# Kernel tuning notes

Measured on AMD Instinct MI355X. Metric: run time of the kernel, lower is better.

The kernel has to match this reference:

```python
import jax, jax.numpy as jnp
import numpy as np

N = 50000  # nodes
E = 800000  # edges (avg degree 16)


def gcn_agg(x, senders, receivers, n, add_self_edges):
    """jraph.GraphConvolution aggregation with symmetric normalization.
    x: [n, d] node feats already passed through update_node_fn."""
    if add_self_edges:
        idx = jnp.arange(n, dtype=senders.dtype)
        s = jnp.concatenate([senders, idx])
        r = jnp.concatenate([receivers, idx])
    else:
        s, r = senders, receivers
    ones = jnp.ones(s.shape, x.dtype)
    sdeg = jax.ops.segment_sum(ones, s, num_segments=n)
    rdeg = jax.ops.segment_sum(ones, r, num_segments=n)
    x = x * jax.lax.rsqrt(jnp.maximum(sdeg, 1.0))[:, None]
    x = jax.ops.segment_sum(x[s], r, num_segments=n)  # [E+,d] gather -> scatter-sum
    return x * jax.lax.rsqrt(jnp.maximum(rdeg, 1.0))[:, None]


def setup_inputs() -> dict:
    key = jax.random.key(0)
    ks = jax.random.split(key, 9)
    d_in, d_h, d_z, d_out = 128, 128, 64, 128

    def w(k, i, o):
        return jax.random.normal(k, (i, o), jnp.float32) / np.float32(np.sqrt(i))

    return {
        "nodes": jax.random.normal(ks[0], (N, d_in), jnp.float32),
        "senders": jax.random.randint(ks[1], (E,), 0, N, jnp.int32),
        "receivers": jax.random.randint(ks[2], (E,), 0, N, jnp.int32),
        "eps": jax.random.normal(ks[3], (N, d_z), jnp.float32),
        "W_h": w(ks[4], d_in, d_h), "b_h": jnp.zeros((d_h,), jnp.float32),
        "W_mu": w(ks[5], d_h, d_z), "b_mu": jnp.zeros((d_z,), jnp.float32),
        "W_ls": w(ks[6], d_h, d_z), "b_ls": jnp.zeros((d_z,), jnp.float32),
        "W_dh": w(ks[7], d_z, d_h), "b_dh": jnp.zeros((d_h,), jnp.float32),
        "W_do": w(ks[8], d_h, d_out), "b_do": jnp.zeros((d_out,), jnp.float32),
    }


def reference(nodes, senders, receivers, eps, W_h, b_h, W_mu, b_mu,
              W_ls, b_ls, W_dh, b_dh, W_do, b_do):
    n = nodes.shape[0]
    # encoder hidden GCN (add_self_edges=True): Linear+elu update, then agg.
    # (the first of the two identical encoder GCN calls in the source is dead
    #  code -- both read the original graph, only the 2nd result is used)
    h = jax.nn.elu(nodes @ W_h + b_h)
    h = gcn_agg(h, senders, receivers, n, True)
    # mean / log_std GCNs (add_self_edges=False)
    mean = gcn_agg(h @ W_mu + b_mu, senders, receivers, n, False)
    log_std = gcn_agg(h @ W_ls + b_ls, senders, receivers, n, False)
    # reparameterization
    z = mean + jnp.exp(log_std) * eps
    # decoder: GCN(self edges, Linear+elu) -> GCN(no self edges, Linear)
    d = jax.nn.elu(z @ W_dh + b_dh)
    d = gcn_agg(d, senders, receivers, n, True)
    out = gcn_agg(d @ W_do + b_do, senders, receivers, n, False)
    return mean, log_std, out
```

## Files before the change

kernel.cpp:

```cpp
#include <hip/hip_runtime.h>
#include <hip/hip_bf16.h>
#include <hip/hip_fp16.h>
#include <math.h>


typedef _Float16 f16x8 __attribute__((ext_vector_type(8)));
typedef float    f32x4 __attribute__((ext_vector_type(4)));

#define HSL 64
#define HIST_LDS_W 12544
#define NSLICE 256
#define CAP 8000

__global__ __launch_bounds__(256)
void hist8s_k(const int* __restrict__ snd, unsigned int* __restrict__ partial,
              int nE, int nW)
{
    __shared__ unsigned int sh[HIST_LDS_W];
    const int slice = blockIdx.x;
    for (int w = threadIdx.x; w < nW; w += 256) sh[w] = 0u;
    __syncthreads();
    const int per = (nE + HSL - 1) / HSL;
    const int e1 = min(nE, slice * per + per);
    for (int e = slice * per + threadIdx.x; e < e1; e += 256) {
        int v = snd[e];
        atomicAdd(&sh[v >> 2], 1u << ((v & 3) * 8));
    }
    __syncthreads();
    unsigned int* dst = partial + (size_t)slice * nW;
    for (int w = threadIdx.x; w < nW; w += 256) dst[w] = sh[w];
}

__global__ __launch_bounds__(256)
void hist8s_reduce_k(const unsigned int* __restrict__ partial,
                     float* __restrict__ dsi, float* __restrict__ dsn,
                     int n, int nW)
{
    int w = blockIdx.x * 256 + threadIdx.x;
    if (w >= nW) return;
    const unsigned int* src = partial + w;
    int c0 = 0, c1 = 0, c2 = 0, c3 = 0;
    for (int s = 0; s < HSL; ++s) {
        unsigned int v = src[(size_t)s * nW];
        c0 += v & 255u; c1 += (v >> 8) & 255u; c2 += (v >> 16) & 255u; c3 += v >> 24;
    }
    const int cc[4] = {c0, c1, c2, c3};
    const int node0 = w * 4;
#pragma unroll
    for (int u = 0; u < 4; ++u) {
        int node = node0 + u;
        if (node >= n) break;
        float fd = (float)cc[u];
        dsi[node] = rsqrtf(fd + 1.0f);
        dsn[node] = rsqrtf(fmaxf(fd, 1.0f));
    }
}

__global__ __launch_bounds__(256)
void rcount_k(const int* __restrict__ rcv, int* __restrict__ cnt, int nE, int nb)
{
    __shared__ int lc[256];
    const int s = blockIdx.x;
    if (threadIdx.x < nb) lc[threadIdx.x] = 0;
    __syncthreads();
    const int per = (nE + NSLICE - 1) / NSLICE;
    const int e1 = min(nE, (s + 1) * per);
    for (int e = s * per + threadIdx.x; e < e1; e += 256)
        atomicAdd(&lc[rcv[e] >> 8], 1);
    __syncthreads();
    if (threadIdx.x < nb) cnt[s * nb + threadIdx.x] = lc[threadIdx.x];
}

__global__ __launch_bounds__(256)
void rscan_k(const int* __restrict__ cnt, int* __restrict__ sbase,
             int* __restrict__ btot, int nb)
{
    __shared__ int sh[256];
    const int b = blockIdx.x, t = threadIdx.x;
    int v = cnt[t * nb + b];
    sh[t] = v; __syncthreads();
#pragma unroll
    for (int off = 1; off < 256; off <<= 1) {
        int u = (t >= off) ? sh[t - off] : 0;
        __syncthreads(); sh[t] += u; __syncthreads();
    }
    sbase[t * nb + b] = sh[t] - v;
    if (t == 255) btot[b] = sh[255];
}

__global__ __launch_bounds__(256)
void rscatter_k(const int* __restrict__ snd, const int* __restrict__ rcv,
                const int* __restrict__ sbase, int2* __restrict__ stage,
                int nE, int nb)
{
    __shared__ int cur[256];
    const int s = blockIdx.x;
    if (threadIdx.x < nb) cur[threadIdx.x] = sbase[s * nb + threadIdx.x];
    __syncthreads();
    const int per = (nE + NSLICE - 1) / NSLICE;
    const int e1 = min(nE, (s + 1) * per);
    for (int e = s * per + threadIdx.x; e < e1; e += 256) {
        int r = rcv[e], b = r >> 8;
        int t = atomicAdd(&cur[b], 1);
        if (t < CAP) stage[(size_t)b * CAP + t] = make_int2(snd[e], r);
    }
}

__global__ __launch_bounds__(256)
void rdeg_k(const int2* __restrict__ stage, const int* __restrict__ btot,
            int* __restrict__ rdeg, float* __restrict__ dri,
            float* __restrict__ drn, int n)
{
    __shared__ int cnt[256];
    const int b = blockIdx.x;
    cnt[threadIdx.x] = 0;
    __syncthreads();
    const int tot = min(btot[b], CAP);
    const int2* sp = stage + (size_t)b * CAP;
    for (int i = threadIdx.x; i < tot; i += 256)
        atomicAdd(&cnt[sp[i].y & 255], 1);
    __syncthreads();
    const int v = b * 256 + threadIdx.x;
    if (v < n) {
        int c = cnt[threadIdx.x];
        rdeg[v] = c;
        float fd = (float)c;
        dri[v] = rsqrtf(fd + 1.0f);
        drn[v] = rsqrtf(fmaxf(fd, 1.0f));
    }
}

__global__ __launch_bounds__(256)
void rsort_k(const int2* __restrict__ stage, const int* __restrict__ btot,
             const int* __restrict__ row_start, int* __restrict__ csr, int n)
{
    __shared__ int loc[256];
    __shared__ int lbuf[CAP];
    const int b = blockIdx.x;
    const int v0 = b * 256;
    const int bstart = row_start[v0 < n ? v0 : n];
    {
        int v = v0 + threadIdx.x;
        loc[threadIdx.x] = row_start[v < n ? v : n] - bstart;
    }
    __syncthreads();
    const int tot = min(btot[b], CAP);
    const int2* sp = stage + (size_t)b * CAP;
    for (int i = threadIdx.x; i < tot; i += 256) {
        int2 p = sp[i];
        int t = atomicAdd(&loc[p.y & 255], 1);
        if (t < CAP) lbuf[t] = p.x;
    }
    __syncthreads();
    for (int i = threadIdx.x; i < tot; i += 256)
        csr[bstart + i] = lbuf[i];
}

__global__ __launch_bounds__(256)
void scan_part_k(const int* __restrict__ deg, int* __restrict__ partial, int n)
{
    __shared__ int sh[256];
    const int t = threadIdx.x;
    const int i = blockIdx.x * 1024 + t * 4;
    int s = 0;
    if (i + 3 < n) { int4 v = *(const int4*)&deg[i]; s = v.x + v.y + v.z + v.w; }
    else { for (int u = 0; u < 4; u++) if (i + u < n) s += deg[i + u]; }
    sh[t] = s; __syncthreads();
    for (int off = 128; off > 0; off >>= 1) {
        if (t < off) sh[t] += sh[t + off];
        __syncthreads();
    }
    if (t == 0) partial[blockIdx.x] = sh[0];
}

__global__ __launch_bounds__(256)
void scan_mid_k(int* __restrict__ partial, int nb, int* __restrict__ row_start, int n)
{
    __shared__ int sh[256];
    const int t = threadIdx.x;
    int v = (t < nb) ? partial[t] : 0;
    sh[t] = v; __syncthreads();
#pragma unroll
    for (int off = 1; off < 256; off <<= 1) {
        int u = (t >= off) ? sh[t - off] : 0;
        __syncthreads();
        sh[t] += u;
        __syncthreads();
    }
    if (t < nb) partial[t] = sh[t];
    if (t == 255) row_start[n] = sh[255];
}

__global__ __launch_bounds__(256)
void scan_apply_k(const int* __restrict__ deg, const int* __restrict__ partial,
                  int* __restrict__ row_start, int n)
{
    __shared__ int sh[256];
    const int t = threadIdx.x;
    const int b = blockIdx.x;
    const int i = b * 1024 + t * 4;
    const int boff = (b == 0) ? 0 : partial[b - 1];
    int v0 = 0, v1 = 0, v2 = 0, v3 = 0;
    if (i + 3 < n) { int4 v = *(const int4*)&deg[i]; v0 = v.x; v1 = v.y; v2 = v.z; v3 = v.w; }
    else {
        if (i     < n) v0 = deg[i];
        if (i + 1 < n) v1 = deg[i + 1];
        if (i + 2 < n) v2 = deg[i + 2];
        if (i + 3 < n) v3 = deg[i + 3];
    }
    const int ts = v0 + v1 + v2 + v3;
    sh[t] = ts; __syncthreads();
#pragma unroll
    for (int off = 1; off < 256; off <<= 1) {
        int u = (t >= off) ? sh[t - off] : 0;
        __syncthreads();
        sh[t] += u;
        __syncthreads();
    }
    const int excl = boff + sh[t] - ts;
    const int p0 = excl, p1 = p0 + v0, p2 = p1 + v1, p3 = p2 + v2;
    if (i + 3 < n) {
        *(int4*)&row_start[i] = make_int4(p0, p1, p2, p3);
    } else {
        if (i     < n) row_start[i]     = p0;
        if (i + 1 < n) row_start[i + 1] = p1;
        if (i + 2 < n) row_start[i + 2] = p2;
        if (i + 3 < n) row_start[i + 3] = p3;
    }
}

__global__ __launch_bounds__(256)
void wprep_k(const float* __restrict__ W_h, const float* __restrict__ W_mu,
             const float* __restrict__ W_ls, const float* __restrict__ W_dh,
             const float* __restrict__ W_do,
             const float* __restrict__ b_mu, const float* __restrict__ b_ls,
             __half* __restrict__ WT_h, __half* __restrict__ WT2,
             __half* __restrict__ WT_dh, __half* __restrict__ WT_do,
             float* __restrict__ bias2)
{
    int gid = blockIdx.x * 256 + threadIdx.x;
    if (gid < 16384) {
        int m = gid >> 7, k = gid & 127;
        WT_h[gid] = __float2half(W_h[k * 128 + m]);
    } else if (gid < 32768) {
        int t = gid - 16384; int m = t >> 7, k = t & 127;
        float v = (m < 64) ? W_mu[k * 64 + m] : W_ls[k * 64 + (m - 64)];
        WT2[t] = __float2half(v);
    } else if (gid < 40960) {
        int t = gid - 32768; int m = t >> 6, k = t & 63;
        WT_dh[t] = __float2half(W_dh[k * 128 + m]);
    } else if (gid < 57344) {
        int t = gid - 40960; int m = t >> 7, k = t & 127;
        WT_do[t] = __float2half(W_do[k * 128 + m]);
    } else if (gid < 57472) {
        int c = gid - 57344;
        bias2[c] = (c < 64) ? b_mu[c] : b_ls[c - 64];
    }
}

template<int K, int ELU, typename XT>
__global__ __launch_bounds__(256)
void mgemm_k(const XT* __restrict__ X, const __half* __restrict__ WT,
             const float* __restrict__ Bias, const float* __restrict__ rowscale,
             __half* __restrict__ Y, int nrows)
{
    const int lane = threadIdx.x & 63;
    const int w    = threadIdx.x >> 6;
    const int l15  = lane & 15, l4 = lane >> 4;
    const int rowbase = blockIdx.x * 128 + w * 32;
    if (rowbase >= nrows) return;

    f32x4 acc[2][8];
#pragma unroll
    for (int mt = 0; mt < 2; ++mt)
#pragma unroll
        for (int nt = 0; nt < 8; ++nt)
#pragma unroll
            for (int q = 0; q < 4; ++q) acc[mt][nt][q] = 0.f;

    const int r0 = min(rowbase + l15,      nrows - 1);
    const int r1 = min(rowbase + 16 + l15, nrows - 1);

#pragma unroll
    for (int ks = 0; ks < K / 32; ++ks) {
        const int ko = ks * 32 + l4 * 8;
        f16x8 a0, a1;
        if constexpr (sizeof(XT) == 4) {
            const float4 p0 = *(const float4*)&X[(size_t)r0 * K + ko];
            const float4 p1 = *(const float4*)&X[(size_t)r0 * K + ko + 4];
            const float4 q0 = *(const float4*)&X[(size_t)r1 * K + ko];
            const float4 q1 = *(const float4*)&X[(size_t)r1 * K + ko + 4];
            a0[0] = (_Float16)p0.x; a0[1] = (_Float16)p0.y;
            a0[2] = (_Float16)p0.z; a0[3] = (_Float16)p0.w;
            a0[4] = (_Float16)p1.x; a0[5] = (_Float16)p1.y;
            a0[6] = (_Float16)p1.z; a0[7] = (_Float16)p1.w;
            a1[0] = (_Float16)q0.x; a1[1] = (_Float16)q0.y;
            a1[2] = (_Float16)q0.z; a1[3] = (_Float16)q0.w;
            a1[4] = (_Float16)q1.x; a1[5] = (_Float16)q1.y;
            a1[6] = (_Float16)q1.z; a1[7] = (_Float16)q1.w;
        } else {
            a0 = *(const f16x8*)&X[(size_t)r0 * K + ko];
            a1 = *(const f16x8*)&X[(size_t)r1 * K + ko];
        }
#pragma unroll
        for (int nt = 0; nt < 8; ++nt) {
            const f16x8 b = *(const f16x8*)&WT[(size_t)(nt * 16 + l15) * K + ko];
            acc[0][nt] = __builtin_amdgcn_mfma_f32_16x16x32_f16(a0, b, acc[0][nt], 0, 0, 0);
            acc[1][nt] = __builtin_amdgcn_mfma_f32_16x16x32_f16(a1, b, acc[1][nt], 0, 0, 0);
        }
    }

    float rs[2][4]; int gr[2][4];
#pragma unroll
    for (int mt = 0; mt < 2; ++mt)
#pragma unroll
        for (int i = 0; i < 4; ++i) {
            int g = rowbase + mt * 16 + l4 * 4 + i;
            gr[mt][i] = g;
            rs[mt][i] = (g < nrows) ? rowscale[g] : 0.f;
        }
#pragma unroll
    for (int nt = 0; nt < 8; ++nt) {
        const float bias = Bias[nt * 16 + l15];
#pragma unroll
        for (int mt = 0; mt < 2; ++mt)
#pragma unroll
            for (int i = 0; i < 4; ++i) {
                if (gr[mt][i] < nrows) {
                    float v = acc[mt][nt][i] + bias;
                    if (ELU) v = (v > 0.f) ? v : expm1f(v);
                    Y[(size_t)gr[mt][i] * 128 + nt * 16 + l15] = __float2half(v * rs[mt][i]);
                }
            }
    }
}

__device__ inline void agg_core(const __half* __restrict__ y, const int* __restrict__ csr,
                                int beg, int end, int g, int c16, float (&acc)[8])
{
    int j = beg;
    for (; j + 8 <= end; j += 8) {
        const int s0 = csr[j + g], s1 = csr[j + 4 + g];
        const f16x8 r0 = *(const f16x8*)&y[(size_t)s0 * 128 + c16 * 8];
        const f16x8 r1 = *(const f16x8*)&y[(size_t)s1 * 128 + c16 * 8];
#pragma unroll
        for (int k = 0; k < 8; ++k) acc[k] += (float)r0[k] + (float)r1[k];
    }
    for (; j < end; j += 4) {
        const int e = j + g;
        const bool ok = e < end;
        const int s = csr[ok ? e : end - 1];
        const f16x8 r = *(const f16x8*)&y[(size_t)s * 128 + c16 * 8];
        if (ok) {
#pragma unroll
            for (int k = 0; k < 8; ++k) acc[k] += (float)r[k];
        }
    }
#pragma unroll
    for (int k = 0; k < 8; ++k) {
        acc[k] += __shfl_xor(acc[k], 16);
        acc[k] += __shfl_xor(acc[k], 32);
    }
}

__global__ __launch_bounds__(256)
void aggw_self_k(const __half* __restrict__ y, const int* __restrict__ row_start,
                 const int* __restrict__ csr, const float* __restrict__ rsc,
                 __half* __restrict__ out, int n)
{
    const int v    = (blockIdx.x * 256 + threadIdx.x) >> 6;
    const int lane = threadIdx.x & 63;
    if (v >= n) return;
    const int g = lane >> 4, c16 = lane & 15;
    const int beg = row_start[v], end = row_start[v + 1];

    float acc[8] = {0.f, 0.f, 0.f, 0.f, 0.f, 0.f, 0.f, 0.f};
    if (g == 0) {
        const f16x8 r = *(const f16x8*)&y[(size_t)v * 128 + c16 * 8];
#pragma unroll
        for (int k = 0; k < 8; ++k) acc[k] += (float)r[k];
    }
    agg_core(y, csr, beg, end, g, c16, acc);
    if (g == 0) {
        const float sc = rsc[v];
        f16x8 o;
#pragma unroll
        for (int k = 0; k < 8; ++k) o[k] = (_Float16)(acc[k] * sc);
        *(f16x8*)&out[(size_t)v * 128 + c16 * 8] = o;
    }
}

__global__ __launch_bounds__(256)
void aggw_f32_k(const __half* __restrict__ y, const int* __restrict__ row_start,
                const int* __restrict__ csr, const float* __restrict__ rsc,
                float* __restrict__ out, int n)
{
    const int v    = (blockIdx.x * 256 + threadIdx.x) >> 6;
    const int lane = threadIdx.x & 63;
    if (v >= n) return;
    const int g = lane >> 4, c16 = lane & 15;
    const int beg = row_start[v], end = row_start[v + 1];

    float acc[8] = {0.f, 0.f, 0.f, 0.f, 0.f, 0.f, 0.f, 0.f};
    agg_core(y, csr, beg, end, g, c16, acc);
    const float sc = rsc[v];
    if (g == 0)
        *(float4*)&out[(size_t)v * 128 + c16 * 8] =
            make_float4(acc[0] * sc, acc[1] * sc, acc[2] * sc, acc[3] * sc);
    if (g == 1)
        *(float4*)&out[(size_t)v * 128 + c16 * 8 + 4] =
            make_float4(acc[4] * sc, acc[5] * sc, acc[6] * sc, acc[7] * sc);
}

__global__ __launch_bounds__(256)
void aggw_2z_k(const __half* __restrict__ y, const int* __restrict__ row_start,
               const int* __restrict__ csr, const float* __restrict__ rsc,
               const float* __restrict__ eps,
               float* __restrict__ mean, float* __restrict__ lstd,
               __half* __restrict__ z16, int n)
{
    const int v    = (blockIdx.x * 256 + threadIdx.x) >> 6;
    const int lane = threadIdx.x & 63;
    if (v >= n) return;
    const int g = lane >> 4, c16 = lane & 15;
    const int beg = row_start[v], end = row_start[v + 1];

    float acc[8] = {0.f, 0.f, 0.f, 0.f, 0.f, 0.f, 0.f, 0.f};
    agg_core(y, csr, beg, end, g, c16, acc);
    const float sc = rsc[v];
#pragma unroll
    for (int k = 0; k < 8; ++k) acc[k] *= sc;

    if (c16 < 8) {
        if (g == 0) *(float4*)&mean[(size_t)v * 64 + c16 * 8]     = make_float4(acc[0], acc[1], acc[2], acc[3]);
        if (g == 1) *(float4*)&mean[(size_t)v * 64 + c16 * 8 + 4] = make_float4(acc[4], acc[5], acc[6], acc[7]);
    } else {
        if (g == 0) *(float4*)&lstd[(size_t)v * 64 + (c16 - 8) * 8]     = make_float4(acc[0], acc[1], acc[2], acc[3]);
        if (g == 1) *(float4*)&lstd[(size_t)v * 64 + (c16 - 8) * 8 + 4] = make_float4(acc[4], acc[5], acc[6], acc[7]);
    }
    float lsv[8];
#pragma unroll
    for (int k = 0; k < 8; ++k) lsv[k] = __shfl_xor(acc[k], 8);
    if (g == 0 && c16 < 8) {
        const float4 e0 = *(const float4*)&eps[(size_t)v * 64 + c16 * 8];
        const float4 e1 = *(const float4*)&eps[(size_t)v * 64 + c16 * 8 + 4];
        const float ev[8] = {e0.x, e0.y, e0.z, e0.w, e1.x, e1.y, e1.z, e1.w};
        f16x8 o;
#pragma unroll
        for (int k = 0; k < 8; ++k) o[k] = (_Float16)(acc[k] + expf(lsv[k]) * ev[k]);
        *(f16x8*)&z16[(size_t)v * 64 + c16 * 8] = o;
    }
}

extern "C" void kernel_launch(void* const* d_in, const int* in_sizes, int n_in,
                              void* d_out, int out_size, void* d_ws, size_t ws_size,
                              hipStream_t stream)
{
    const float* nodes = (const float*)d_in[0];
    const int*   snd   = (const int*)d_in[1];
    const int*   rcv   = (const int*)d_in[2];
    const float* eps   = (const float*)d_in[3];
    const float* W_h  = (const float*)d_in[4];  const float* b_h  = (const float*)d_in[5];
    const float* W_mu = (const float*)d_in[6];  const float* b_mu = (const float*)d_in[7];
    const float* W_ls = (const float*)d_in[8];  const float* b_ls = (const float*)d_in[9];
    const float* W_dh = (const float*)d_in[10]; const float* b_dh = (const float*)d_in[11];
    const float* W_do = (const float*)d_in[12]; const float* b_do = (const float*)d_in[13];

    const int n  = in_sizes[0] / 128;
    const int nE = in_sizes[1];
    const int nW = (n + 3) >> 2;
    const int nb = (n + 255) >> 8;

    __half* bufA16 = (__half*)d_ws;
    __half* bufB16 = bufA16 + (size_t)n * 128;
    __half* bufC16 = bufB16 + (size_t)n * 128;
    float* dsi = (float*)(bufC16 + (size_t)n * 64);
    float* dri = dsi + n;
    float* dsn = dri + n;
    float* drn = dsn + n;
    int* rdeg      = (int*)(drn + n);
    int* row_start = rdeg + n;
    int* spart     = row_start + n + 4;
    int* csr       = spart + 256;
    int* cnt       = csr + nE;
    int* sbase     = cnt + 256 * nb;
    int* btot      = sbase + 256 * nb;
    __half* WT_h  = (__half*)(btot + 256);
    __half* WT2   = WT_h + 16384;
    __half* WT_dh = WT2 + 16384;
    __half* WT_do = WT_dh + 8192;
    float*  bias2 = (float*)(WT_do + 16384);
    unsigned int* partial = (unsigned int*)bufA16;
    int2* stage = (int2*)bufB16;

    float* mean = (float*)d_out;
    float* lstd = mean + (size_t)n * 64;
    float* outp = lstd + (size_t)n * 64;

    auto cdiv = [](int a, int b) { return (a + b - 1) / b; };
    const int gG = cdiv(n, 128);
    const int gW = cdiv(n * 64, 256);
    const int sb = cdiv(n, 1024);

    wprep_k<<<cdiv(57472, 256), 256, 0, stream>>>(W_h, W_mu, W_ls, W_dh, W_do,
                                                  b_mu, b_ls, WT_h, WT2, WT_dh, WT_do, bias2);
    hist8s_k<<<HSL, 256, 0, stream>>>(snd, partial, nE, nW);
    hist8s_reduce_k<<<cdiv(nW, 256), 256, 0, stream>>>(partial, dsi, dsn, n, nW);
    rcount_k<<<NSLICE, 256, 0, stream>>>(rcv, cnt, nE, nb);
    rscan_k<<<nb, 256, 0, stream>>>(cnt, sbase, btot, nb);
    rscatter_k<<<NSLICE, 256, 0, stream>>>(snd, rcv, sbase, stage, nE, nb);
    rdeg_k<<<nb, 256, 0, stream>>>(stage, btot, rdeg, dri, drn, n);
    scan_part_k<<<sb, 256, 0, stream>>>(rdeg, spart, n);
    scan_mid_k<<<1, 256, 0, stream>>>(spart, sb, row_start, n);
    scan_apply_k<<<sb, 256, 0, stream>>>(rdeg, spart, row_start, n);
    rsort_k<<<nb, 256, 0, stream>>>(stage, btot, row_start, csr, n);

    mgemm_k<128, 1, float><<<gG, 256, 0, stream>>>(nodes, WT_h, b_h, dsi, bufA16, n);
    aggw_self_k<<<gW, 256, 0, stream>>>(bufA16, row_start, csr, dri, bufB16, n);

    mgemm_k<128, 0, __half><<<gG, 256, 0, stream>>>(bufB16, WT2, bias2, dsn, bufA16, n);
    aggw_2z_k<<<gW, 256, 0, stream>>>(bufA16, row_start, csr, drn, eps, mean, lstd, bufC16, n);

    mgemm_k<64, 1, __half><<<gG, 256, 0, stream>>>(bufC16, WT_dh, b_dh, dsi, bufA16, n);
    aggw_self_k<<<gW, 256, 0, stream>>>(bufA16, row_start, csr, dri, bufB16, n);

    mgemm_k<128, 0, __half><<<gG, 256, 0, stream>>>(bufB16, WT_do, b_do, dsn, bufA16, n);
    aggw_f32_k<<<gW, 256, 0, stream>>>(bufA16, row_start, csr, drn, outp, n);
}
```

Measured before the change: 309.8 us.

## Store byte offsets in CSR and unroll gather-aggregation with packed half2 adds

The CSR build now stores each sender index pre-shifted by 8, so it is a byte offset into the 256-byte fp16 row. The aggregation kernels can then load rows without a multiply. The aggregation core gains a 16-edge unrolled loop that issues four independent 16-byte gathers per lane, pairs rows with packed half2 adds, and accumulates in float2. This aims for more memory-level parallelism and fewer conversion instructions per gathered row. The cost is that pairs of neighbour rows are summed in fp16 before widening to fp32, which adds some rounding error. The int byte offsets also limit node count to about 8M.

```diff
diff --git a/kernel.cpp b/kernel.cpp
--- a/kernel.cpp
+++ b/kernel.cpp
@@ -6,6 +6,8 @@
 
 typedef _Float16 f16x8 __attribute__((ext_vector_type(8)));
 typedef float    f32x4 __attribute__((ext_vector_type(4)));
+
+union H2x4 { int4 i; __half2 h[4]; };
 
 #define HSL 64
 #define HIST_LDS_W 12544
@@ -153,7 +155,7 @@
     }
     __syncthreads();
     for (int i = threadIdx.x; i < tot; i += 256)
-        csr[bstart + i] = lbuf[i];
+        csr[bstart + i] = lbuf[i] << 8;
 }
 
 __global__ __launch_bounds__(256)
@@ -335,31 +337,58 @@
     }
 }
 
-__device__ inline void agg_core(const __half* __restrict__ y, const int* __restrict__ csr,
-                                int beg, int end, int g, int c16, float (&acc)[8])
+__device__ inline void agg_core(const char* __restrict__ yb, const int* __restrict__ csr,
+                                int beg, int end, int g, float2 (&acc)[4])
 {
     int j = beg;
+    for (; j + 16 <= end; j += 16) {
+        const int o0 = csr[j + g], o1 = csr[j + 4 + g];
+        const int o2 = csr[j + 8 + g], o3 = csr[j + 12 + g];
+        H2x4 r0, r1, r2, r3;
+        r0.i = *(const int4*)(yb + o0);
+        r1.i = *(const int4*)(yb + o1);
+        r2.i = *(const int4*)(yb + o2);
+        r3.i = *(const int4*)(yb + o3);
+#pragma unroll
+        for (int k = 0; k < 4; ++k) {
+            const float2 f01 = __half22float2(__hadd2(r0.h[k], r1.h[k]));
+            const float2 f23 = __half22float2(__hadd2(r2.h[k], r3.h[k]));
+            acc[k].x += f01.x + f23.x;
+            acc[k].y += f01.y + f23.y;
+        }
+    }
     for (; j + 8 <= end; j += 8) {
-        const int s0 = csr[j + g], s1 = csr[j + 4 + g];
-        const f16x8 r0 = *(const f16x8*)&y[(size_t)s0 * 128 + c16 * 8];
-        const f16x8 r1 = *(const f16x8*)&y[(size_t)s1 * 128 + c16 * 8];
-#pragma unroll
-        for (int k = 0; k < 8; ++k) acc[k] += (float)r0[k] + (float)r1[k];
+        const int o0 = csr[j + g], o1 = csr[j + 4 + g];
+        H2x4 r0, r1;
+        r0.i = *(const int4*)(yb + o0);
+        r1.i = *(const int4*)(yb + o1);
+#pragma unroll
+        for (int k = 0; k < 4; ++k) {
+            const float2 f01 = __half22float2(__hadd2(r0.h[k], r1.h[k]));
+            acc[k].x += f01.x;
+            acc[k].y += f01.y;
+        }
     }
     for (; j < end; j += 4) {
         const int e = j + g;
         const bool ok = e < end;
-        const int s = csr[ok ? e : end - 1];
-        const f16x8 r = *(const f16x8*)&y[(size_t)s * 128 + c16 * 8];
+        const int o = csr[ok ? e : end - 1];
+        H2x4 r; r.i = *(const int4*)(yb + o);
         if (ok) {
 #pragma unroll
-            for (int k = 0; k < 8; ++k) acc[k] += (float)r[k];
-        }
-    }
-#pragma unroll
-    for (int k = 0; k < 8; ++k) {
-        acc[k] += __shfl_xor(acc[k], 16);
-        acc[k] += __shfl_xor(acc[k], 32);
+            for (int k = 0; k < 4; ++k) {
+                const float2 f = __half22float2(r.h[k]);
+                acc[k].x += f.x;
+                acc[k].y += f.y;
+            }
+        }
+    }
+#pragma unroll
+    for (int k = 0; k < 4; ++k) {
+        acc[k].x += __shfl_xor(acc[k].x, 16);
+        acc[k].y += __shfl_xor(acc[k].y, 16);
+        acc[k].x += __shfl_xor(acc[k].x, 32);
+        acc[k].y += __shfl_xor(acc[k].y, 32);
     }
 }
 
@@ -373,19 +402,26 @@
     if (v >= n) return;
     const int g = lane >> 4, c16 = lane & 15;
     const int beg = row_start[v], end = row_start[v + 1];
-
-    float acc[8] = {0.f, 0.f, 0.f, 0.f, 0.f, 0.f, 0.f, 0.f};
+    const char* yb = (const char*)y + c16 * 16;
+
+    float2 acc[4] = {{0.f,0.f},{0.f,0.f},{0.f,0.f},{0.f,0.f}};
     if (g == 0) {
-        const f16x8 r = *(const f16x8*)&y[(size_t)v * 128 + c16 * 8];
-#pragma unroll
-        for (int k = 0; k < 8; ++k) acc[k] += (float)r[k];
-    }
-    agg_core(y, csr, beg, end, g, c16, acc);
+        H2x4 r; r.i = *(const int4*)(yb + (v << 8));
+#pragma unroll
+        for (int k = 0; k < 4; ++k) {
+            const float2 f = __half22float2(r.h[k]);
+            acc[k].x += f.x; acc[k].y += f.y;
+        }
+    }
+    agg_core(yb, csr, beg, end, g, acc);
     if (g == 0) {
         const float sc = rsc[v];
         f16x8 o;
 #pragma unroll
-        for (int k = 0; k < 8; ++k) o[k] = (_Float16)(acc[k] * sc);
+        for (int k = 0; k < 4; ++k) {
+            o[2 * k]     = (_Float16)(acc[k].x * sc);
+            o[2 * k + 1] = (_Float16)(acc[k].y * sc);
+        }
         *(f16x8*)&out[(size_t)v * 128 + c16 * 8] = o;
     }
 }
@@ -400,16 +436,17 @@
     if (v >= n) return;
     const int g = lane >> 4, c16 = lane & 15;
     const int beg = row_start[v], end = row_start[v + 1];
-
-    float acc[8] = {0.f, 0.f, 0.f, 0.f, 0.f, 0.f, 0.f, 0.f};
-    agg_core(y, csr, beg, end, g, c16, acc);
+    const char* yb = (const char*)y + c16 * 16;
+
+    float2 acc[4] = {{0.f,0.f},{0.f,0.f},{0.f,0.f},{0.f,0.f}};
+    agg_core(yb, csr, beg, end, g, acc);
     const float sc = rsc[v];
     if (g == 0)
         *(float4*)&out[(size_t)v * 128 + c16 * 8] =
-            make_float4(acc[0] * sc, acc[1] * sc, acc[2] * sc, acc[3] * sc);
+            make_float4(acc[0].x * sc, acc[0].y * sc, acc[1].x * sc, acc[1].y * sc);
     if (g == 1)
         *(float4*)&out[(size_t)v * 128 + c16 * 8 + 4] =
-            make_float4(acc[4] * sc, acc[5] * sc, acc[6] * sc, acc[7] * sc);
+            make_float4(acc[2].x * sc, acc[2].y * sc, acc[3].x * sc, acc[3].y * sc);
 }
 
 __global__ __launch_bounds__(256)
@@ -424,12 +461,17 @@
     if (v >= n) return;
     const int g = lane >> 4, c16 = lane & 15;
     const int beg = row_start[v], end = row_start[v + 1];
-
-    float acc[8] = {0.f, 0.f, 0.f, 0.f, 0.f, 0.f, 0.f, 0.f};
-    agg_core(y, csr, beg, end, g, c16, acc);
+    const char* yb = (const char*)y + c16 * 16;
+
+    float2 acc2[4] = {{0.f,0.f},{0.f,0.f},{0.f,0.f},{0.f,0.f}};
+    agg_core(yb, csr, beg, end, g, acc2);
     const float sc = rsc[v];
-#pragma unroll
-    for (int k = 0; k < 8; ++k) acc[k] *= sc;
+    float acc[8];
+#pragma unroll
+    for (int k = 0; k < 4; ++k) {
+        acc[2 * k]     = acc2[k].x * sc;
+        acc[2 * k + 1] = acc2[k].y * sc;
+    }
 
     if (c16 < 8) {
         if (g == 0) *(float4*)&mean[(size_t)v * 64 + c16 * 8]     = make_float4(acc[0], acc[1], acc[2], acc[3]);
```

Result: no change. 304.3 us (-1.8%).
